# Kernel tuning notes

Measured on AMD Instinct MI355X. Metric: run time of the kernel, lower is better.

Reference implementation:

```python
import jax, jax.numpy as jnp
import numpy as np

B, D, H, W, C = 2, 8, 128, 128, 64
HEADS, DH = 4, 16
EPS = 1e-12  # torch F.normalize eps


def setup_inputs() -> dict:
    key = jax.random.key(0)
    ks = jax.random.split(key, 8)
    rn = lambda k, shp, s: jax.random.normal(k, shp, jnp.float32) * s
    return {
        "x_in": rn(ks[0], (B, D, H, W, C), 1.0),
        "Wq": rn(ks[1], (C, HEADS * DH), 0.05),
        "Wk": rn(ks[2], (C, HEADS * DH), 0.05),
        "Wv": rn(ks[3], (C, HEADS * DH), 0.05),
        "rescale": jnp.ones((HEADS, 1, 1), jnp.float32),
        "Wproj": rn(ks[4], (HEADS * DH, C), 0.05),
        "bproj": jnp.zeros((C,), jnp.float32),
        "Wpos1": rn(ks[5], (C, 1, 3, 3, 3), 0.1),
        "Wpos2": rn(ks[6], (C, 1, 3, 3, 3), 0.1),
    }


def _l2norm(x):
    # torch F.normalize(p=2, dim=-1): x / max(||x||, eps)
    return x / jnp.maximum(jnp.linalg.norm(x, axis=-1, keepdims=True), EPS)


def _dwconv3d(x, w):
    # depthwise Conv3d, kernel 3, stride 1, padding 1, groups = channels
    return jax.lax.conv_general_dilated(
        x, w, (1, 1, 1), 'SAME',
        dimension_numbers=('NCDHW', 'OIDHW', 'NCDHW'),
        feature_group_count=w.shape[0])


def reference(x_in, Wq, Wk, Wv, rescale, Wproj, bproj, Wpos1, Wpos2):
    b, d, h, w, c = x_in.shape
    n = d * h * w
    x = x_in.reshape(b, n, c)
    v_inp = x @ Wv                                   # [b, n, heads*dh]
    # [b, heads, dh, n] layout (attention over channel dim)
    q = jnp.transpose((x @ Wq).reshape(b, n, HEADS, DH), (0, 2, 3, 1))
    k = jnp.transpose((x @ Wk).reshape(b, n, HEADS, DH), (0, 2, 3, 1))
    v = jnp.transpose(v_inp.reshape(b, n, HEADS, DH), (0, 2, 3, 1))
    q = _l2norm(q)
    k = _l2norm(k)
    attn = jnp.einsum('bhdn,bhen->bhde', k, q) * rescale  # [b, heads, dh, dh]
    attn = jax.nn.softmax(attn, axis=-1)
    out = jnp.einsum('bhde,bhen->bhdn', attn, v)          # [b, heads, dh, n]
    out = jnp.transpose(out, (0, 3, 1, 2)).reshape(b, n, HEADS * DH)
    out_c = (out @ Wproj + bproj).reshape(b, d, h, w, c)
    # positional branch: depthwise conv -> GELU -> depthwise conv on v_inp
    vv = jnp.transpose(v_inp.reshape(b, d, h, w, c), (0, 4, 1, 2, 3))  # NCDHW
    p = _dwconv3d(vv, Wpos1)
    p = jax.nn.gelu(p, approximate=False)
    p = _dwconv3d(p, Wpos2)
    out_p = jnp.transpose(p, (0, 2, 3, 4, 1))
    return out_c + out_p
```

## Files before the change

kernel.cpp:

```cpp
#include <hip/hip_runtime.h>
#include <math.h>

#define DD 8
#define HH 128
#define WW2 128
#define NPT 131072
#define NTOT 262144
#define NBK 32

typedef __attribute__((ext_vector_type(8))) short short8;
typedef __attribute__((ext_vector_type(4))) float f32x4;
typedef __attribute__((ext_vector_type(4))) unsigned short u16x4;
typedef __attribute__((ext_vector_type(8))) unsigned short u16x8;
typedef unsigned short u16;

static const size_t OFF_P1  = 0;
static const size_t OFF_P2  = 33554432;
static const size_t OFF_V   = 67108864;
static const size_t OFF_PW  = 100663296;
static const size_t OFF_PM  = 100687872;
static const size_t OFF_FLAG= 100704256;
static const size_t OFF_CW  = 100704768;
#define GP_F    0
#define NKP_F   65536
#define NQP_F   69632
#define NPART_TOT 73728
#define CW_WPROJ 0
#define CW_WPOS1 4096
#define CW_WPOS2 5824
#define CW_RESC  7552
#define CW_BPROJ 7556

__device__ __forceinline__ float bf2f(u16 u){
  unsigned int x = ((unsigned int)u) << 16;
  return __builtin_bit_cast(float, x);
}
__device__ __forceinline__ u16 f2bf(float f){
  unsigned int x = __builtin_bit_cast(unsigned int, f);
  unsigned int r = (x + 0x7fffu + ((x >> 16) & 1u)) >> 16;
  return (u16)r;
}

__global__ __launch_bounds__(256) void k_prep(const void* __restrict__ x,
    const void* __restrict__ Wproj, const void* __restrict__ rescale,
    const void* __restrict__ bproj, const void* __restrict__ Wpos1,
    const void* __restrict__ Wpos2,
    int* __restrict__ flag, float* __restrict__ cw, float* __restrict__ gpart){
  __shared__ int sflag;
  int t = threadIdx.x, blk = blockIdx.x;
  for (int i = blk * 2304 + t; i < (blk + 1) * 2304 && i < NPART_TOT; i += 256)
    gpart[i] = 0.f;
  if (blk != 0) return;
  if (t < 64){
    u16 u = ((const u16*)x)[2 * t];
    int e = (u >> 7) & 0xFF;
    int plaus = (u == 0) || (u == 0x8000u) || (e >= 100 && e <= 130);
    unsigned long long m = __ballot(plaus);
    if (t == 0){
      sflag = (__popcll(m) < 48) ? 1 : 0;
      *flag = sflag;
    }
  }
  __syncthreads();
  int isf32 = sflag;
  auto conv = [&](const void* src, float* dst, int n){
    for (int i = t; i < n; i += 256)
      dst[i] = isf32 ? ((const float*)src)[i] : bf2f(((const u16*)src)[i]);
  };
  conv(Wproj, cw + CW_WPROJ, 4096);
  conv(Wpos1, cw + CW_WPOS1, 1728);
  conv(Wpos2, cw + CW_WPOS2, 1728);
  conv(rescale, cw + CW_RESC, 4);
  conv(bproj,   cw + CW_BPROJ, 64);
}

__global__ __launch_bounds__(256) void kpack_w(const void* __restrict__ Wq,
                                               const void* __restrict__ Wk,
                                               const void* __restrict__ Wv,
                                               const int* __restrict__ flag,
                                               u16* __restrict__ packW){
  int isf32 = *flag;
  int o = blockIdx.x * 256 + threadIdx.x;
  int f = o >> 9, l = (o >> 3) & 63, j = o & 7;
  int tt = f >> 1, s = f & 1;
  int k = s * 32 + (l >> 4) * 8 + j;
  int n = tt * 16 + (l & 15);
  const void* W = (n < 64) ? Wq : (n < 128) ? Wk : Wv;
  int idx = k * 64 + (n & 63);
  float val = isf32 ? ((const float*)W)[idx] : bf2f(((const u16*)W)[idx]);
  packW[o] = f2bf(val);
}

__device__ __forceinline__ short8 ld8_adapt(const void* p, size_t idx, int isf32){
  if (!isf32) return *(const short8*)((const u16*)p + idx);
  const float4* f = (const float4*)((const float*)p + idx);
  float4 u = f[0], v2 = f[1];
  short8 r;
  r[0] = (short)f2bf(u.x);  r[1] = (short)f2bf(u.y);
  r[2] = (short)f2bf(u.z);  r[3] = (short)f2bf(u.w);
  r[4] = (short)f2bf(v2.x); r[5] = (short)f2bf(v2.y);
  r[6] = (short)f2bf(v2.z); r[7] = (short)f2bf(v2.w);
  return r;
}

__global__ __launch_bounds__(256) void k_qkv(const void* __restrict__ x, const int* __restrict__ flag,
                                             const u16* __restrict__ packW, u16* __restrict__ vT,
                                             float* __restrict__ Gp, float* __restrict__ NkP,
                                             float* __restrict__ NqP){
  __shared__ u16 sK[64][72];
  __shared__ u16 sQ[64][72];
  int isf32 = *flag;
  int wave = threadIdx.x >> 6, lane = threadIdx.x & 63;
  int m = lane & 15, quad = lane >> 4;
  int p0 = blockIdx.x * 64 + wave * 16;
  size_t rowbase = (size_t)(p0 + m) * 64;
  short8 a0 = ld8_adapt(x, rowbase + quad * 8, isf32);
  short8 a1 = ld8_adapt(x, rowbase + 32 + quad * 8, isf32);
  const short8* bw = (const short8*)packW;
  f32x4 acc[12];
#pragma unroll
  for (int t = 0; t < 12; t++) acc[t] = (f32x4)(0.f);
#pragma unroll
  for (int t = 0; t < 12; t++){
    short8 b0 = bw[(t * 2 + 0) * 64 + lane];
    short8 b1 = bw[(t * 2 + 1) * 64 + lane];
    acc[t] = __builtin_amdgcn_mfma_f32_16x16x32_bf16(a0, b0, acc[t], 0, 0, 0);
    acc[t] = __builtin_amdgcn_mfma_f32_16x16x32_bf16(a1, b1, acc[t], 0, 0, 0);
  }
  int b = p0 >> 17;
  int nloc = p0 & (NPT - 1);
  int pl = wave * 16 + quad * 4;
#pragma unroll
  for (int t = 0; t < 4; t++){
    u16x4 pk;
#pragma unroll
    for (int r = 0; r < 4; r++) pk[r] = f2bf(acc[t][r]);
    *(u16x4*)&sQ[t * 16 + m][pl] = pk;
  }
#pragma unroll
  for (int t = 4; t < 8; t++){
    u16x4 pk;
#pragma unroll
    for (int r = 0; r < 4; r++) pk[r] = f2bf(acc[t][r]);
    *(u16x4*)&sK[(t - 4) * 16 + m][pl] = pk;
  }
#pragma unroll
  for (int t = 8; t < 12; t++){
    int ch = (t - 8) * 16 + m;
    u16x4 pk;
#pragma unroll
    for (int r = 0; r < 4; r++) pk[r] = f2bf(acc[t][r]);
    *(u16x4*)(vT + ((size_t)(b * 64 + ch)) * NPT + nloc + quad * 4) = pk;
  }
  __syncthreads();
  int h = wave;
  f32x4 aG = (f32x4)(0.f), aKK = (f32x4)(0.f), aQQ = (f32x4)(0.f);
#pragma unroll
  for (int cc = 0; cc < 2; cc++){
    short8 kf = *(const short8*)&sK[h * 16 + m][cc * 32 + quad * 8];
    short8 qf = *(const short8*)&sQ[h * 16 + m][cc * 32 + quad * 8];
    aG  = __builtin_amdgcn_mfma_f32_16x16x32_bf16(kf, qf, aG, 0, 0, 0);
    aKK = __builtin_amdgcn_mfma_f32_16x16x32_bf16(kf, kf, aKK, 0, 0, 0);
    aQQ = __builtin_amdgcn_mfma_f32_16x16x32_bf16(qf, qf, aQQ, 0, 0, 0);
  }
  int bk = blockIdx.x & (NBK - 1);
  float* Gb = Gp + ((size_t)(bk * 2 + b) * 4 + h) * 256;
#pragma unroll
  for (int r = 0; r < 4; r++){
    int d = quad * 4 + r, e = m;
    atomicAdd(&Gb[d * 16 + e], aG[r]);
    if (d == e){
      atomicAdd(&NkP[(bk * 2 + b) * 64 + h * 16 + d], aKK[r]);
      atomicAdd(&NqP[(bk * 2 + b) * 64 + h * 16 + d], aQQ[r]);
    }
  }
}

__global__ __launch_bounds__(256) void k_attn(const float* __restrict__ Gp, const float* __restrict__ NkP,
                                              const float* __restrict__ NqP, const float* __restrict__ cw,
                                              u16* __restrict__ packM){
  __shared__ float sG[1024];
  __shared__ float sNk[64], sNq[64];
  __shared__ float sA[4][16][16];
  __shared__ float sM[64][64];
  __shared__ float sWp[64][64];
  int b = blockIdx.x, t = threadIdx.x;
  for (int i = t; i < 1024; i += 256){
    float s = 0.f;
    for (int bk = 0; bk < NBK; bk++) s += Gp[(size_t)(bk * 2 + b) * 1024 + i];
    sG[i] = s;
  }
  if (t < 64){
    float s1 = 0.f, s2 = 0.f;
    for (int bk = 0; bk < NBK; bk++){
      s1 += NkP[(bk * 2 + b) * 64 + t];
      s2 += NqP[(bk * 2 + b) * 64 + t];
    }
    sNk[t] = s1; sNq[t] = s2;
  }
  for (int i = t; i < 4096; i += 256) sWp[i >> 6][i & 63] = cw[CW_WPROJ + i];
  __syncthreads();
  if (t < 64){
    int h = t >> 4, d = t & 15;
    float nk = fmaxf(sqrtf(sNk[t]), 1e-12f);
    float rs = cw[CW_RESC + h];
    float lg[16]; float mx = -1e30f;
#pragma unroll
    for (int e = 0; e < 16; e++){
      float nq = fmaxf(sqrtf(sNq[h * 16 + e]), 1e-12f);
      float L = sG[h * 256 + d * 16 + e] / (nk * nq) * rs;
      lg[e] = L; mx = fmaxf(mx, L);
    }
    float sum = 0.f;
#pragma unroll
    for (int e = 0; e < 16; e++){ lg[e] = expf(lg[e] - mx); sum += lg[e]; }
    float inv = 1.f / sum;
#pragma unroll
    for (int e = 0; e < 16; e++) sA[h][d][e] = lg[e] * inv;
  }
  __syncthreads();
  for (int i = t; i < 4096; i += 256){
    int he = i >> 6, c = i & 63;
    int h = he >> 4, e = he & 15;
    float acc = 0.f;
#pragma unroll
    for (int d = 0; d < 16; d++) acc += sA[h][d][e] * sWp[h * 16 + d][c];
    sM[he][c] = acc;
  }
  __syncthreads();
  for (int i = t; i < 4096; i += 256){
    int f = i >> 9, l = (i >> 3) & 63, j = i & 7;
    int t4 = f >> 1, s = f & 1;
    int k = s * 32 + (l >> 4) * 8 + j;
    int n = t4 * 16 + (l & 15);
    packM[b * 4096 + i] = f2bf(sM[k][n]);
  }
}

template <bool GELU>
__global__ __launch_bounds__(256) void k_dwconv(const u16* __restrict__ src, const float* __restrict__ wpos,
                                                u16* __restrict__ dst){
  int xi = threadIdx.x & 15, ty = threadIdx.x >> 4;
  int x0 = xi * 8;
  int c  = blockIdx.x;
  int z  = blockIdx.y >> 3;
  int y  = (blockIdx.y & 7) * 16 + ty;
  int b  = blockIdx.z;
  float wgt[27];
#pragma unroll
  for (int i = 0; i < 27; i++) wgt[i] = wpos[c * 27 + i];
  const u16* plane = src + (size_t)(b * 64 + c) * NPT;
  float acc[8];
#pragma unroll
  for (int i = 0; i < 8; i++) acc[i] = 0.f;
#pragma unroll
  for (int kd = 0; kd < 3; kd++){
    int zz = z - 1 + kd;
    if (zz < 0 || zz >= DD) continue;
#pragma unroll
    for (int kh = 0; kh < 3; kh++){
      int yyr = y - 1 + kh;
      int yc = yyr < 0 ? 0 : (yyr > HH - 1 ? HH - 1 : yyr);
      float vmask = (yyr == yc) ? 1.f : 0.f;
      const u16* rp = plane + zz * 16384 + yc * 128 + x0;
      short8 mid = *(const short8*)rp;
      u16 lft = 0, rgt = 0;
      if (x0 > 0)   lft = rp[-1];
      if (x0 < 120) rgt = rp[8];
      float row[10];
      row[0] = bf2f(lft);
#pragma unroll
      for (int e = 0; e < 8; e++) row[1 + e] = bf2f((u16)mid[e]);
      row[9] = bf2f(rgt);
#pragma unroll
      for (int kw = 0; kw < 3; kw++){
        float w = wgt[kd * 9 + kh * 3 + kw] * vmask;
#pragma unroll
        for (int xx = 0; xx < 8; xx++)
          acc[xx] = fmaf(row[xx + kw], w, acc[xx]);
      }
    }
  }
  u16x8 pk;
#pragma unroll
  for (int xx = 0; xx < 8; xx++){
    float o = acc[xx];
    if (GELU) o = 0.5f * o * (1.f + erff(o * 0.70710678118654752f));
    pk[xx] = f2bf(o);
  }
  *(u16x8*)(dst + (size_t)(b * 64 + c) * NPT + z * 16384 + y * 128 + x0) = pk;
}

__global__ __launch_bounds__(256) void k_final(const u16* __restrict__ vT, const u16* __restrict__ packM,
                                               const float* __restrict__ bprojf, const u16* __restrict__ p2T,
                                               float* __restrict__ out){
  int wave = threadIdx.x >> 6, lane = threadIdx.x & 63;
  int m = lane & 15, quad = lane >> 4;
  int p0 = blockIdx.x * 64 + wave * 16;
  int b = p0 >> 17;
  int nloc = p0 & (NPT - 1);
  short8 a0, a1;
#pragma unroll
  for (int j = 0; j < 8; j++){
    a0[j] = (short)vT[(size_t)(b * 64 + quad * 8 + j) * NPT + nloc + m];
    a1[j] = (short)vT[(size_t)(b * 64 + 32 + quad * 8 + j) * NPT + nloc + m];
  }
  const short8* bm = (const short8*)(packM + (size_t)b * 4096);
  f32x4 acc[4];
#pragma unroll
  for (int t = 0; t < 4; t++) acc[t] = (f32x4)(0.f);
#pragma unroll
  for (int t = 0; t < 4; t++){
    short8 b0 = bm[(t * 2 + 0) * 64 + lane];
    short8 b1 = bm[(t * 2 + 1) * 64 + lane];
    acc[t] = __builtin_amdgcn_mfma_f32_16x16x32_bf16(a0, b0, acc[t], 0, 0, 0);
    acc[t] = __builtin_amdgcn_mfma_f32_16x16x32_bf16(a1, b1, acc[t], 0, 0, 0);
  }
#pragma unroll
  for (int t = 0; t < 4; t++){
    int c = t * 16 + m;
    float bias = bprojf[c];
    u16x4 pv = *(const u16x4*)(p2T + (size_t)(b * 64 + c) * NPT + nloc + quad * 4);
#pragma unroll
    for (int r = 0; r < 4; r++){
      size_t p = (size_t)p0 + quad * 4 + r;
      out[p * 64 + c] = acc[t][r] + bias + bf2f(pv[r]);
    }
  }
}

extern "C" void kernel_launch(void* const* d_in, const int* in_sizes, int n_in,
                              void* d_out, int out_size, void* d_ws, size_t ws_size,
                              hipStream_t stream){
  (void)in_sizes; (void)n_in; (void)out_size; (void)ws_size;
  const void* x      = d_in[0];
  const void* Wq     = d_in[1];
  const void* Wk     = d_in[2];
  const void* Wv     = d_in[3];
  const void* rescale= d_in[4];
  const void* Wproj  = d_in[5];
  const void* bproj  = d_in[6];
  const void* Wpos1  = d_in[7];
  const void* Wpos2  = d_in[8];

  char* ws = (char*)d_ws;
  u16* p1T   = (u16*)(ws + OFF_P1);
  u16* p2T   = (u16*)(ws + OFF_P2);
  u16* vT    = (u16*)(ws + OFF_V);
  u16* packW = (u16*)(ws + OFF_PW);
  u16* packM = (u16*)(ws + OFF_PM);
  int* flag  = (int*)(ws + OFF_FLAG);
  float* cw  = (float*)(ws + OFF_CW);
  float* Gp  = (float*)(ws + OFF_P1) + GP_F;
  float* NkP = (float*)(ws + OFF_P1) + NKP_F;
  float* NqP = (float*)(ws + OFF_P1) + NQP_F;
  float* out = (float*)d_out;

  k_prep<<<32, 256, 0, stream>>>(x, Wproj, rescale, bproj, Wpos1, Wpos2, flag, cw, Gp);
  kpack_w<<<48, 256, 0, stream>>>(Wq, Wk, Wv, flag, packW);
  k_qkv<<<NTOT / 64, 256, 0, stream>>>(x, flag, packW, vT, Gp, NkP, NqP);
  k_attn<<<2, 256, 0, stream>>>(Gp, NkP, NqP, cw, packM);
  k_dwconv<true><<<dim3(64, 64, 2), 256, 0, stream>>>(vT, cw + CW_WPOS1, p1T);
  k_dwconv<false><<<dim3(64, 64, 2), 256, 0, stream>>>(p1T, cw + CW_WPOS2, p2T);
  k_final<<<NTOT / 64, 256, 0, stream>>>(vT, packM, cw + CW_BPROJ, p2T, out);
}
```

Measured before the change: 302.7 us.

## Compute attention Gram via input covariance X^T X instead of Q/K projections

Instead of projecting Q and K per pixel and accumulating K·Q^T plus the norms, the QKV kernel now accumulates the 64x64 input covariance X^T X per batch. The attention kernel derives the Gram matrix and the Q/K norms from it through Wq and Wk. This removes the Q/K MFMAs and their shared-memory staging from the bandwidth-heavy pass, and each 512-thread block now covers 512 pixels, so fewer atomics are issued. In exchange, the single-block attention kernel does more serial matmul work, and the Q/K values are never rounded to bf16, which changes numerics slightly.

```diff
diff --git a/kernel.cpp b/kernel.cpp
--- a/kernel.cpp
+++ b/kernel.cpp
@@ -21,10 +21,10 @@
 static const size_t OFF_PM  = 100687872;
 static const size_t OFF_FLAG= 100704256;
 static const size_t OFF_CW  = 100704768;
-#define GP_F    0
-#define NKP_F   65536
-#define NQP_F   69632
-#define NPART_TOT 73728
+#define SP_F    0
+#define WQ_F    262144
+#define WK_F    266240
+#define NPART_TOT 262144
 #define CW_WPROJ 0
 #define CW_WPOS1 4096
 #define CW_WPOS2 5824
@@ -44,11 +44,12 @@
 __global__ __launch_bounds__(256) void k_prep(const void* __restrict__ x,
     const void* __restrict__ Wproj, const void* __restrict__ rescale,
     const void* __restrict__ bproj, const void* __restrict__ Wpos1,
-    const void* __restrict__ Wpos2,
+    const void* __restrict__ Wpos2, const void* __restrict__ Wq,
+    const void* __restrict__ Wk,
     int* __restrict__ flag, float* __restrict__ cw, float* __restrict__ gpart){
   __shared__ int sflag;
   int t = threadIdx.x, blk = blockIdx.x;
-  for (int i = blk * 2304 + t; i < (blk + 1) * 2304 && i < NPART_TOT; i += 256)
+  for (int i = blk * 8192 + t; i < (blk + 1) * 8192; i += 256)
     gpart[i] = 0.f;
   if (blk != 0) return;
   if (t < 64){
@@ -72,11 +73,11 @@
   conv(Wpos2, cw + CW_WPOS2, 1728);
   conv(rescale, cw + CW_RESC, 4);
   conv(bproj,   cw + CW_BPROJ, 64);
-}
-
-__global__ __launch_bounds__(256) void kpack_w(const void* __restrict__ Wq,
-                                               const void* __restrict__ Wk,
-                                               const void* __restrict__ Wv,
+  conv(Wq, gpart + WQ_F, 4096);
+  conv(Wk, gpart + WK_F, 4096);
+}
+
+__global__ __launch_bounds__(256) void kpack_w(const void* __restrict__ Wv,
                                                const int* __restrict__ flag,
                                                u16* __restrict__ packW){
   int isf32 = *flag;
@@ -85,9 +86,8 @@
   int tt = f >> 1, s = f & 1;
   int k = s * 32 + (l >> 4) * 8 + j;
   int n = tt * 16 + (l & 15);
-  const void* W = (n < 64) ? Wq : (n < 128) ? Wk : Wv;
-  int idx = k * 64 + (n & 63);
-  float val = isf32 ? ((const float*)W)[idx] : bf2f(((const u16*)W)[idx]);
+  int idx = k * 64 + n;
+  float val = isf32 ? ((const float*)Wv)[idx] : bf2f(((const u16*)Wv)[idx]);
   packW[o] = f2bf(val);
 }
 
@@ -103,103 +103,129 @@
   return r;
 }
 
-__global__ __launch_bounds__(256) void k_qkv(const void* __restrict__ x, const int* __restrict__ flag,
-                                             const u16* __restrict__ packW, u16* __restrict__ vT,
-                                             float* __restrict__ Gp, float* __restrict__ NkP,
-                                             float* __restrict__ NqP){
-  __shared__ u16 sK[64][72];
-  __shared__ u16 sQ[64][72];
+__global__ __launch_bounds__(512) void k_qkv(const void* __restrict__ x,
+                                             const int* __restrict__ flag,
+                                             const u16* __restrict__ packW,
+                                             u16* __restrict__ vT,
+                                             float* __restrict__ Sp){
+  __shared__ u16 sXT[64][136];
   int isf32 = *flag;
   int wave = threadIdx.x >> 6, lane = threadIdx.x & 63;
   int m = lane & 15, quad = lane >> 4;
-  int p0 = blockIdx.x * 64 + wave * 16;
-  size_t rowbase = (size_t)(p0 + m) * 64;
-  short8 a0 = ld8_adapt(x, rowbase + quad * 8, isf32);
-  short8 a1 = ld8_adapt(x, rowbase + 32 + quad * 8, isf32);
   const short8* bw = (const short8*)packW;
-  f32x4 acc[12];
-#pragma unroll
-  for (int t = 0; t < 12; t++) acc[t] = (f32x4)(0.f);
-#pragma unroll
-  for (int t = 0; t < 12; t++){
-    short8 b0 = bw[(t * 2 + 0) * 64 + lane];
-    short8 b1 = bw[(t * 2 + 1) * 64 + lane];
-    acc[t] = __builtin_amdgcn_mfma_f32_16x16x32_bf16(a0, b0, acc[t], 0, 0, 0);
-    acc[t] = __builtin_amdgcn_mfma_f32_16x16x32_bf16(a1, b1, acc[t], 0, 0, 0);
-  }
-  int b = p0 >> 17;
-  int nloc = p0 & (NPT - 1);
-  int pl = wave * 16 + quad * 4;
-#pragma unroll
-  for (int t = 0; t < 4; t++){
-    u16x4 pk;
-#pragma unroll
-    for (int r = 0; r < 4; r++) pk[r] = f2bf(acc[t][r]);
-    *(u16x4*)&sQ[t * 16 + m][pl] = pk;
-  }
-#pragma unroll
-  for (int t = 4; t < 8; t++){
-    u16x4 pk;
-#pragma unroll
-    for (int r = 0; r < 4; r++) pk[r] = f2bf(acc[t][r]);
-    *(u16x4*)&sK[(t - 4) * 16 + m][pl] = pk;
-  }
-#pragma unroll
-  for (int t = 8; t < 12; t++){
-    int ch = (t - 8) * 16 + m;
-    u16x4 pk;
-#pragma unroll
-    for (int r = 0; r < 4; r++) pk[r] = f2bf(acc[t][r]);
-    *(u16x4*)(vT + ((size_t)(b * 64 + ch)) * NPT + nloc + quad * 4) = pk;
-  }
-  __syncthreads();
-  int h = wave;
-  f32x4 aG = (f32x4)(0.f), aKK = (f32x4)(0.f), aQQ = (f32x4)(0.f);
-#pragma unroll
-  for (int cc = 0; cc < 2; cc++){
-    short8 kf = *(const short8*)&sK[h * 16 + m][cc * 32 + quad * 8];
-    short8 qf = *(const short8*)&sQ[h * 16 + m][cc * 32 + quad * 8];
-    aG  = __builtin_amdgcn_mfma_f32_16x16x32_bf16(kf, qf, aG, 0, 0, 0);
-    aKK = __builtin_amdgcn_mfma_f32_16x16x32_bf16(kf, kf, aKK, 0, 0, 0);
-    aQQ = __builtin_amdgcn_mfma_f32_16x16x32_bf16(qf, qf, aQQ, 0, 0, 0);
+  short8 bv[8];
+#pragma unroll
+  for (int f = 0; f < 8; f++) bv[f] = bw[f * 64 + lane];
+  int c1 = wave >> 1, c2p = (wave & 1) * 2;
+  f32x4 aS[2];
+  aS[0] = (f32x4)(0.f); aS[1] = (f32x4)(0.f);
+
+  int pbase = blockIdx.x * 512;
+  int b = pbase >> 17;
+
+  for (int s = 0; s < 4; s++){
+    int p0 = pbase + s * 128 + wave * 16;
+    size_t rowbase = (size_t)(p0 + m) * 64;
+    short8 a0 = ld8_adapt(x, rowbase + quad * 8, isf32);
+    short8 a1 = ld8_adapt(x, rowbase + 32 + quad * 8, isf32);
+    f32x4 av[4];
+#pragma unroll
+    for (int t = 0; t < 4; t++) av[t] = (f32x4)(0.f);
+#pragma unroll
+    for (int t = 0; t < 4; t++){
+      av[t] = __builtin_amdgcn_mfma_f32_16x16x32_bf16(a0, bv[t * 2 + 0], av[t], 0, 0, 0);
+      av[t] = __builtin_amdgcn_mfma_f32_16x16x32_bf16(a1, bv[t * 2 + 1], av[t], 0, 0, 0);
+    }
+    int nloc = p0 & (NPT - 1);
+#pragma unroll
+    for (int t = 0; t < 4; t++){
+      u16x4 pk;
+#pragma unroll
+      for (int r = 0; r < 4; r++) pk[r] = f2bf(av[t][r]);
+      *(u16x4*)(vT + ((size_t)(b * 64 + t * 16 + m)) * NPT + nloc + quad * 4) = pk;
+    }
+    if (s) __syncthreads();
+#pragma unroll
+    for (int j = 0; j < 8; j++){
+      sXT[quad * 8 + j][wave * 16 + m]      = (u16)a0[j];
+      sXT[32 + quad * 8 + j][wave * 16 + m] = (u16)a1[j];
+    }
+    __syncthreads();
+#pragma unroll
+    for (int ks = 0; ks < 4; ks++){
+      short8 fA  = *(const short8*)&sXT[c1 * 16 + m][ks * 32 + quad * 8];
+      short8 fB0 = *(const short8*)&sXT[(c2p + 0) * 16 + m][ks * 32 + quad * 8];
+      short8 fB1 = *(const short8*)&sXT[(c2p + 1) * 16 + m][ks * 32 + quad * 8];
+      aS[0] = __builtin_amdgcn_mfma_f32_16x16x32_bf16(fA, fB0, aS[0], 0, 0, 0);
+      aS[1] = __builtin_amdgcn_mfma_f32_16x16x32_bf16(fA, fB1, aS[1], 0, 0, 0);
+    }
   }
   int bk = blockIdx.x & (NBK - 1);
-  float* Gb = Gp + ((size_t)(bk * 2 + b) * 4 + h) * 256;
-#pragma unroll
-  for (int r = 0; r < 4; r++){
-    int d = quad * 4 + r, e = m;
-    atomicAdd(&Gb[d * 16 + e], aG[r]);
-    if (d == e){
-      atomicAdd(&NkP[(bk * 2 + b) * 64 + h * 16 + d], aKK[r]);
-      atomicAdd(&NqP[(bk * 2 + b) * 64 + h * 16 + d], aQQ[r]);
-    }
-  }
-}
-
-__global__ __launch_bounds__(256) void k_attn(const float* __restrict__ Gp, const float* __restrict__ NkP,
-                                              const float* __restrict__ NqP, const float* __restrict__ cw,
+  float* Sb = Sp + (size_t)(bk * 2 + b) * 4096;
+#pragma unroll
+  for (int tt = 0; tt < 2; tt++)
+#pragma unroll
+    for (int r = 0; r < 4; r++)
+      atomicAdd(&Sb[(c1 * 16 + quad * 4 + r) * 64 + (c2p + tt) * 16 + m], aS[tt][r]);
+}
+
+__global__ __launch_bounds__(256) void k_attn(const float* __restrict__ Sp,
+                                              const float* __restrict__ wqk,
+                                              const float* __restrict__ cw,
                                               u16* __restrict__ packM){
+  __shared__ float sS[4096];
+  __shared__ float sW[4096];
+  __shared__ float sU[4096];
   __shared__ float sG[1024];
-  __shared__ float sNk[64], sNq[64];
-  __shared__ float sA[4][16][16];
-  __shared__ float sM[64][64];
-  __shared__ float sWp[64][64];
+  __shared__ float sA[1024];
+  __shared__ float sNq[64], sNk[64];
   int b = blockIdx.x, t = threadIdx.x;
+  for (int i = t; i < 4096; i += 256){
+    float s = 0.f;
+    for (int bk = 0; bk < NBK; bk++) s += Sp[(size_t)(bk * 2 + b) * 4096 + i];
+    sS[i] = s;
+    sW[i] = wqk[i];
+  }
+  __syncthreads();
+  for (int i = t; i < 4096; i += 256){
+    int cc = i >> 6, e = i & 63;
+    float acc = 0.f;
+#pragma unroll 8
+    for (int c2 = 0; c2 < 64; c2++) acc += sS[cc * 64 + c2] * sW[c2 * 64 + e];
+    sU[i] = acc;
+  }
+  __syncthreads();
+  if (t < 64){
+    float a = 0.f;
+    for (int c = 0; c < 64; c++) a += sW[c * 64 + t] * sU[c * 64 + t];
+    sNq[t] = a;
+  }
+  __syncthreads();
+  for (int i = t; i < 4096; i += 256) sW[i] = wqk[4096 + i];
+  __syncthreads();
   for (int i = t; i < 1024; i += 256){
-    float s = 0.f;
-    for (int bk = 0; bk < NBK; bk++) s += Gp[(size_t)(bk * 2 + b) * 1024 + i];
-    sG[i] = s;
-  }
+    int h = i >> 8, d = (i >> 4) & 15, e = i & 15;
+    float acc = 0.f;
+#pragma unroll 8
+    for (int c = 0; c < 64; c++) acc += sW[c * 64 + h * 16 + d] * sU[c * 64 + h * 16 + e];
+    sG[i] = acc;
+  }
+  __syncthreads();
+  for (int i = t; i < 4096; i += 256){
+    int cc = i >> 6, e = i & 63;
+    float acc = 0.f;
+#pragma unroll 8
+    for (int c2 = 0; c2 < 64; c2++) acc += sS[cc * 64 + c2] * sW[c2 * 64 + e];
+    sU[i] = acc;
+  }
+  __syncthreads();
   if (t < 64){
-    float s1 = 0.f, s2 = 0.f;
-    for (int bk = 0; bk < NBK; bk++){
-      s1 += NkP[(bk * 2 + b) * 64 + t];
-      s2 += NqP[(bk * 2 + b) * 64 + t];
-    }
-    sNk[t] = s1; sNq[t] = s2;
-  }
-  for (int i = t; i < 4096; i += 256) sWp[i >> 6][i & 63] = cw[CW_WPROJ + i];
-  __syncthreads();
+    float a = 0.f;
+    for (int c = 0; c < 64; c++) a += sW[c * 64 + t] * sU[c * 64 + t];
+    sNk[t] = a;
+  }
+  __syncthreads();
+  for (int i = t; i < 4096; i += 256) sW[i] = cw[CW_WPROJ + i];
   if (t < 64){
     int h = t >> 4, d = t & 15;
     float nk = fmaxf(sqrtf(sNk[t]), 1e-12f);
@@ -216,7 +242,7 @@
     for (int e = 0; e < 16; e++){ lg[e] = expf(lg[e] - mx); sum += lg[e]; }
     float inv = 1.f / sum;
 #pragma unroll
-    for (int e = 0; e < 16; e++) sA[h][d][e] = lg[e] * inv;
+    for (int e = 0; e < 16; e++) sA[h * 256 + d * 16 + e] = lg[e] * inv;
   }
   __syncthreads();
   for (int i = t; i < 4096; i += 256){
@@ -224,16 +250,16 @@
     int h = he >> 4, e = he & 15;
     float acc = 0.f;
 #pragma unroll
-    for (int d = 0; d < 16; d++) acc += sA[h][d][e] * sWp[h * 16 + d][c];
-    sM[he][c] = acc;
+    for (int d = 0; d < 16; d++) acc += sA[h * 256 + d * 16 + e] * sW[(h * 16 + d) * 64 + c];
+    sU[i] = acc;
   }
   __syncthreads();
   for (int i = t; i < 4096; i += 256){
     int f = i >> 9, l = (i >> 3) & 63, j = i & 7;
-    int t4 = f >> 1, s = f & 1;
-    int k = s * 32 + (l >> 4) * 8 + j;
+    int t4 = f >> 1, s2 = f & 1;
+    int k = s2 * 32 + (l >> 4) * 8 + j;
     int n = t4 * 16 + (l & 15);
-    packM[b * 4096 + i] = f2bf(sM[k][n]);
+    packM[b * 4096 + i] = f2bf(sU[k * 64 + n]);
   }
 }
 
@@ -351,15 +377,14 @@
   u16* packM = (u16*)(ws + OFF_PM);
   int* flag  = (int*)(ws + OFF_FLAG);
   float* cw  = (float*)(ws + OFF_CW);
-  float* Gp  = (float*)(ws + OFF_P1) + GP_F;
-  float* NkP = (float*)(ws + OFF_P1) + NKP_F;
-  float* NqP = (float*)(ws + OFF_P1) + NQP_F;
+  float* Sp  = (float*)(ws + OFF_P1) + SP_F;
+  float* wqk = (float*)(ws + OFF_P1) + WQ_F;
   float* out = (float*)d_out;
 
-  k_prep<<<32, 256, 0, stream>>>(x, Wproj, rescale, bproj, Wpos1, Wpos2, flag, cw, Gp);
-  kpack_w<<<48, 256, 0, stream>>>(Wq, Wk, Wv, flag, packW);
-  k_qkv<<<NTOT / 64, 256, 0, stream>>>(x, flag, packW, vT, Gp, NkP, NqP);
-  k_attn<<<2, 256, 0, stream>>>(Gp, NkP, NqP, cw, packM);
+  k_prep<<<32, 256, 0, stream>>>(x, Wproj, rescale, bproj, Wpos1, Wpos2, Wq, Wk, flag, cw, Sp);
+  kpack_w<<<16, 256, 0, stream>>>(Wv, flag, packW);
+  k_qkv<<<NTOT / 512, 512, 0, stream>>>(x, flag, packW, vT, Sp);
+  k_attn<<<2, 256, 0, stream>>>(Sp, wqk, cw, packM);
   k_dwconv<true><<<dim3(64, 64, 2), 256, 0, stream>>>(vT, cw + CW_WPOS1, p1T);
   k_dwconv<false><<<dim3(64, 64, 2), 256, 0, stream>>>(p1T, cw + CW_WPOS2, p2T);
   k_final<<<NTOT / 64, 256, 0, stream>>>(vT, packM, cw + CW_BPROJ, p2T, out);
```

Result: slower. 317.5 us (+4.9%).
